# Kernel optimization log

Measured on AMD Instinct MI355X. Metric: run time of the kernel, lower is better.

## Reference

```python
import jax, jax.numpy as jnp
import numpy as np

B, N, E, H, MAXLEN = 64, 256, 1024, 16, 512
D = E // H
LN_EPS = 1e-5
NORM_EPS = 1e-12


def setup_inputs() -> dict:
    key = jax.random.key(0)
    ks = jax.random.split(key, 12)
    s = 1.0 / np.sqrt(E)
    return {
        "news_embeds": jax.random.normal(ks[0], (B, N, E), jnp.float32),
        "padding_mask": jax.random.uniform(ks[1], (B, N)) > 0.8,  # True = padded
        "cls_token": jax.random.normal(ks[2], (1, 1, E), jnp.float32),
        "pos_emb": jax.random.normal(ks[3], (MAXLEN + 1, E), jnp.float32) * 0.02,
        "in_proj_w": jax.random.normal(ks[4], (3 * E, E), jnp.float32) * s,
        "in_proj_b": jnp.zeros((3 * E,), jnp.float32),
        "out_proj_w": jax.random.normal(ks[5], (E, E), jnp.float32) * s,
        "out_proj_b": jnp.zeros((E,), jnp.float32),
        "proj_w": jax.random.normal(ks[6], (E, E), jnp.float32) * s,
        "proj_b": jnp.zeros((E,), jnp.float32),
        "ln_gamma": jnp.ones((E,), jnp.float32),
        "ln_beta": jnp.zeros((E,), jnp.float32),
    }


def reference(news_embeds, padding_mask, cls_token, pos_emb, in_proj_w, in_proj_b,
              out_proj_w, out_proj_b, proj_w, proj_b, ln_gamma, ln_beta):
    b, n, e = news_embeds.shape
    S = n + 1
    # prepend CLS token, add positional encodings (dropout inactive in eval)
    x = jnp.concatenate([jnp.broadcast_to(cls_token, (b, 1, e)), news_embeds], axis=1)
    x = x + pos_emb[:S][None, :, :]
    # key padding mask with CLS always attendable
    mask = jnp.concatenate(
        [jnp.zeros((b, 1), dtype=bool), padding_mask], axis=1)  # [b,S]
    # packed QKV projection (nn.MultiheadAttention in_proj)
    qkv = jnp.einsum('bse,fe->bsf', x, in_proj_w) + in_proj_b
    q, k, v = jnp.split(qkv, 3, axis=-1)
    q = q.reshape(b, S, H, D)
    k = k.reshape(b, S, H, D)
    v = v.reshape(b, S, H, D)
    scores = jnp.einsum('bqhd,bkhd->bhqk', q, k) / jnp.sqrt(
        jnp.asarray(D, x.dtype))
    big_neg = jnp.asarray(-1e9, scores.dtype)
    scores = jnp.where(mask[:, None, None, :], big_neg, scores)
    attn = jax.nn.softmax(scores, axis=-1)  # [b,H,S,S]
    ctx = jnp.einsum('bhqk,bkhd->bqhd', attn, v).reshape(b, S, e)
    attn_out = jnp.einsum('bse,fe->bsf', ctx, out_proj_w) + out_proj_b
    # projection head: Linear -> (Dropout eval noop) -> LayerNorm -> ReLU
    p = jnp.einsum('bse,fe->bsf', attn_out, proj_w) + proj_b
    mu = jnp.mean(p, axis=-1, keepdims=True)
    var = jnp.var(p, axis=-1, keepdims=True)
    ln = (p - mu) * jax.lax.rsqrt(var + LN_EPS) * ln_gamma + ln_beta
    proj = jax.nn.relu(ln)
    user = proj[:, 0, :]
    norm = jnp.maximum(jnp.linalg.norm(user, axis=-1, keepdims=True), NORM_EPS)
    user = user / norm
    return user, attn
```

## Files before the change

### kernel.cpp

```cpp
#include <hip/hip_runtime.h>

#define B_   64
#define N_   256
#define E_   1024
#define H_   16
#define D_   64
#define S_   257
#define M_   16448
#define MP2  16640
#define N3_  3072
#define K_   1024

typedef unsigned short u16;
typedef unsigned int   u32;
typedef __bf16 bf16x8 __attribute__((ext_vector_type(8)));
typedef float  f32x4  __attribute__((ext_vector_type(4)));

__device__ inline u16 f2bf(float f) {
  union { float f; u32 u; } a; a.f = f;
  return (u16)((a.u + 0x7FFFu + ((a.u >> 16) & 1u)) >> 16);
}
__device__ inline float bf2f(u16 h) {
  union { u32 u; float f; } a; a.u = ((u32)h) << 16; return a.f;
}
__device__ inline void gload_lds16(const void* g, void* l) {
  __builtin_amdgcn_global_load_lds((const __attribute__((address_space(1))) void*)g,
                                   (__attribute__((address_space(3))) void*)l, 16, 0, 0);
}

__global__ __launch_bounds__(256) void prep_w(const float* __restrict__ w, u16* __restrict__ o) {
  size_t i = ((size_t)blockIdx.x * 256 + threadIdx.x) * 4;
  float4 f = *(const float4*)(w + i);
  ushort4 v;
  v.x = f2bf(f.x); v.y = f2bf(f.y); v.z = f2bf(f.z); v.w = f2bf(f.w);
  *(ushort4*)(o + i) = v;
}

__global__ __launch_bounds__(256) void build_x(const float* __restrict__ news,
                                               const float* __restrict__ cls,
                                               const float* __restrict__ pos,
                                               u16* __restrict__ x) {
  const int row = blockIdx.x;
  const int e = threadIdx.x * 4;
  float4 v = make_float4(0.f, 0.f, 0.f, 0.f);
  if (row < M_) {
    const int b = row / S_;
    const int s = row - b * S_;
    float4 pe = *(const float4*)(pos + (size_t)s * E_ + e);
    float4 xv = (s == 0) ? *(const float4*)(cls + e)
                         : *(const float4*)(news + ((size_t)b * N_ + (s - 1)) * E_ + e);
    v.x = xv.x + pe.x; v.y = xv.y + pe.y; v.z = xv.z + pe.z; v.w = xv.w + pe.w;
  }
  ushort4 o;
  o.x = f2bf(v.x); o.y = f2bf(v.y); o.z = f2bf(v.z); o.w = f2bf(v.w);
  *(ushort4*)(x + (size_t)row * E_ + e) = o;
}

__global__ __launch_bounds__(256) void mask_prep(const void* __restrict__ src, int* __restrict__ dst) {
  const int t = threadIdx.x;
  const u32* wsrc = (const u32*)src;
  u32 flag = 0;
  for (int i = t; i < 4096; i += 256) {
    u32 v = wsrc[i];
    if (v == 0x3F800000u) flag |= 2u;
    else if (v > 1u) flag |= 1u;
  }
  __shared__ u32 fsh;
  if (t == 0) fsh = 0;
  __syncthreads();
  if (flag) atomicOr(&fsh, flag);
  __syncthreads();
  const u32 f = fsh;
  const int mode = (f & 2u) ? 2 : ((f & 1u) ? 1 : 0);
  const int base = blockIdx.x * 2048;
  for (int i = base + t; i < base + 2048; i += 256) {
    int m;
    if (mode == 0)      m = (wsrc[i] != 0u);
    else if (mode == 2) m = (((const float*)src)[i] != 0.f);
    else                m = (((const unsigned char*)src)[i] != 0);
    dst[i] = m;
  }
}

__global__ __launch_bounds__(256) void gemm_qkv(const u16* __restrict__ A,
                                                const u16* __restrict__ Bw,
                                                const float* __restrict__ bias,
                                                u16* __restrict__ C) {
  __shared__ u16 As[128 * 32];
  __shared__ u16 Bs[128 * 32];
  const int t = threadIdx.x;
  const int w = t >> 6, l = t & 63;
  const int wr = w >> 1, wc = w & 1;

  const int orig = blockIdx.x;
  const int wgid = (orig & 7) * 390 + (orig >> 3);
  const int bm = wgid / 24, bn = wgid % 24;

  const u16* Ab = A + (size_t)bm * 128 * K_;
  const u16* Bb = Bw + (size_t)bn * 128 * K_;
  f32x4 acc[4][4] = {};
  const int r0 = t >> 2,         col0 = (t & 3) << 3;
  const int r1 = (256 + t) >> 2, col1 = ((256 + t) & 3) << 3;
  char* AsB = (char*)As + w * 1024;
  char* BsB = (char*)Bs + w * 1024;

  for (int k0 = 0; k0 < K_; k0 += 32) {
    gload_lds16(Ab + (size_t)r0 * K_ + k0 + col0, AsB);
    gload_lds16(Ab + (size_t)r1 * K_ + k0 + col1, AsB + 4096);
    gload_lds16(Bb + (size_t)r0 * K_ + k0 + col0, BsB);
    gload_lds16(Bb + (size_t)r1 * K_ + k0 + col1, BsB + 4096);
    __syncthreads();
    const int kc = (l >> 4) << 3;
    bf16x8 af[4], bfr[4];
#pragma unroll
    for (int m = 0; m < 4; ++m)
      af[m] = *(const bf16x8*)&As[(wr * 64 + m * 16 + (l & 15)) * 32 + kc];
#pragma unroll
    for (int n = 0; n < 4; ++n)
      bfr[n] = *(const bf16x8*)&Bs[(wc * 64 + n * 16 + (l & 15)) * 32 + kc];
#pragma unroll
    for (int m = 0; m < 4; ++m)
#pragma unroll
      for (int n = 0; n < 4; ++n)
        acc[m][n] = __builtin_amdgcn_mfma_f32_16x16x32_bf16(af[m], bfr[n], acc[m][n], 0, 0, 0);
    __syncthreads();
  }
  const int row0 = bm * 128 + wr * 64 + ((l >> 4) << 2);
  const int colb = bn * 128 + wc * 64 + (l & 15);
#pragma unroll
  for (int n = 0; n < 4; ++n) {
    const int col = colb + n * 16;
    const float bv = bias[col];
#pragma unroll
    for (int m = 0; m < 4; ++m) {
      const int row = row0 + m * 16;
#pragma unroll
      for (int j = 0; j < 4; ++j)
        C[(size_t)(row + j) * N3_ + col] = f2bf(acc[m][n][j] + bv);
    }
  }
}

__global__ __launch_bounds__(256) void attn_kernel(const u16* __restrict__ qkv,
                                                   const int* __restrict__ maskw,
                                                   float* __restrict__ attn,
                                                   float* __restrict__ ctx) {
  __shared__ float msk[272];
  __shared__ float p0[272];
  __shared__ float red[4][64];
  const int qt = blockIdx.x, h = blockIdx.y, b = blockIdx.z;
  const int t = threadIdx.x;
  const int q0 = qt * 64;

  for (int i = t; i < 272; i += 256) {
    float m = 0.f;
    if (i == 0) m = 1.f;
    else if (i < S_) m = maskw[b * N_ + i - 1] ? 0.f : 1.f;
    msk[i] = m;
  }
  __syncthreads();

  const int w = t >> 6, l = t & 63;
  const int cl = l & 15, rg = l >> 4;
  const int kc = rg * 8;

  const u16* qrow = qkv + (size_t)(b * S_ + q0 + w * 16 + cl) * N3_ + h * 64 + kc;
  const bf16x8 qa0 = *(const bf16x8*)qrow;
  const bf16x8 qa1 = *(const bf16x8*)(qrow + 32);

  const u16* kbase0 = qkv + (size_t)(b * S_) * N3_ + E_ + h * 64 + kc;

  float ev[17][4];
  float sum[4] = {0.f, 0.f, 0.f, 0.f};
#pragma unroll
  for (int kt = 0; kt < 17; ++kt) {
    const u16* kb = kbase0 + (size_t)(kt * 16 + cl) * N3_;
    f32x4 a = {0.f, 0.f, 0.f, 0.f};
    a = __builtin_amdgcn_mfma_f32_16x16x32_bf16(qa0, *(const bf16x8*)kb, a, 0, 0, 0);
    a = __builtin_amdgcn_mfma_f32_16x16x32_bf16(qa1, *(const bf16x8*)(kb + 32), a, 0, 0, 0);
    const float m = msk[kt * 16 + cl];
#pragma unroll
    for (int j = 0; j < 4; ++j) {
      const float e = m * __expf(a[j] * 0.125f);
      ev[kt][j] = e;
      sum[j] += e;
    }
  }
  float inv[4];
#pragma unroll
  for (int j = 0; j < 4; ++j) {
#pragma unroll
    for (int o = 1; o < 16; o <<= 1) sum[j] += __shfl_xor(sum[j], o);
    inv[j] = 1.f / sum[j];
  }

  const int qrow0 = q0 + w * 16 + rg * 4;
  float* abase = attn + (size_t)(b * H_ + h) * S_ * S_;
#pragma unroll
  for (int j = 0; j < 4; ++j) {
    const int gq = qrow0 + j;
    if (gq < S_) {
      float* arow = abase + (size_t)gq * S_;
#pragma unroll
      for (int kt = 0; kt < 17; ++kt) {
        const int col = kt * 16 + cl;
        if (col < S_) arow[col] = ev[kt][j] * inv[j];
      }
    }
  }

  if (qt == 0) {
    if (w == 0 && rg == 0) {
      const float iv = inv[0];
#pragma unroll
      for (int kt = 0; kt < 17; ++kt) p0[kt * 16 + cl] = ev[kt][0] * iv;
    }
    __syncthreads();
    const int part = t >> 6, d = t & 63;
    float acc = 0.f;
    for (int k = part; k < S_; k += 4)
      acc = fmaf(p0[k], bf2f(qkv[(size_t)(b * S_ + k) * N3_ + 2 * E_ + h * 64 + d]), acc);
    red[part][d] = acc;
    __syncthreads();
    if (t < 64)
      ctx[(size_t)b * E_ + h * 64 + t] = red[0][t] + red[1][t] + red[2][t] + red[3][t];
  }
}

__global__ __launch_bounds__(256) void gemv_cls(const float* __restrict__ in,
                                                const float* __restrict__ W,
                                                const float* __restrict__ bias,
                                                float* __restrict__ out) {
  const int bt = blockIdx.x, fc = blockIdx.y, t = threadIdx.x;
  __shared__ float xs[4][E_];
  for (int i = t; i < E_; i += 256)
    ((float4*)xs)[i] = ((const float4*)(in + (size_t)bt * 4 * E_))[i];
  __syncthreads();
  const int f = fc * 64 + (t >> 2);
  const int ec = (t & 3) * 256;
  const float4* wr = (const float4*)(W + (size_t)f * E_ + ec);
  float a0 = 0.f, a1 = 0.f, a2 = 0.f, a3 = 0.f;
#pragma unroll 8
  for (int e4 = 0; e4 < 64; ++e4) {
    const float4 wv = wr[e4];
    const float4 x0 = *(const float4*)&xs[0][ec + e4 * 4];
    const float4 x1 = *(const float4*)&xs[1][ec + e4 * 4];
    const float4 x2 = *(const float4*)&xs[2][ec + e4 * 4];
    const float4 x3 = *(const float4*)&xs[3][ec + e4 * 4];
    a0 += wv.x * x0.x + wv.y * x0.y + wv.z * x0.z + wv.w * x0.w;
    a1 += wv.x * x1.x + wv.y * x1.y + wv.z * x1.z + wv.w * x1.w;
    a2 += wv.x * x2.x + wv.y * x2.y + wv.z * x2.z + wv.w * x2.w;
    a3 += wv.x * x3.x + wv.y * x3.y + wv.z * x3.z + wv.w * x3.w;
  }
  a0 += __shfl_xor(a0, 1); a0 += __shfl_xor(a0, 2);
  a1 += __shfl_xor(a1, 1); a1 += __shfl_xor(a1, 2);
  a2 += __shfl_xor(a2, 1); a2 += __shfl_xor(a2, 2);
  a3 += __shfl_xor(a3, 1); a3 += __shfl_xor(a3, 2);
  if ((t & 3) == 0) {
    const float bv = bias[f];
    out[(size_t)(bt * 4 + 0) * E_ + f] = a0 + bv;
    out[(size_t)(bt * 4 + 1) * E_ + f] = a1 + bv;
    out[(size_t)(bt * 4 + 2) * E_ + f] = a2 + bv;
    out[(size_t)(bt * 4 + 3) * E_ + f] = a3 + bv;
  }
}

__global__ __launch_bounds__(256) void ln_relu_norm(const float* __restrict__ p,
                                                    const float* __restrict__ gamma,
                                                    const float* __restrict__ beta,
                                                    float* __restrict__ user) {
  const int b = blockIdx.x, t = threadIdx.x;
  const int w = t >> 6, l = t & 63;
  const float4 v = ((const float4*)(p + (size_t)b * E_))[t];
  float s = v.x + v.y + v.z + v.w;
  float s2 = v.x * v.x + v.y * v.y + v.z * v.z + v.w * v.w;
#pragma unroll
  for (int o = 1; o < 64; o <<= 1) { s += __shfl_xor(s, o); s2 += __shfl_xor(s2, o); }
  __shared__ float ss[4], ss2[4], qs[4];
  if (l == 0) { ss[w] = s; ss2[w] = s2; }
  __syncthreads();
  s = ss[0] + ss[1] + ss[2] + ss[3];
  s2 = ss2[0] + ss2[1] + ss2[2] + ss2[3];
  const float mu = s * (1.f / E_);
  const float var = s2 * (1.f / E_) - mu * mu;
  const float rstd = rsqrtf(var + 1e-5f);
  const float4 g = ((const float4*)gamma)[t];
  const float4 be = ((const float4*)beta)[t];
  float4 o;
  o.x = fmaxf((v.x - mu) * rstd * g.x + be.x, 0.f);
  o.y = fmaxf((v.y - mu) * rstd * g.y + be.y, 0.f);
  o.z = fmaxf((v.z - mu) * rstd * g.z + be.z, 0.f);
  o.w = fmaxf((v.w - mu) * rstd * g.w + be.w, 0.f);
  float q2 = o.x * o.x + o.y * o.y + o.z * o.z + o.w * o.w;
#pragma unroll
  for (int off = 1; off < 64; off <<= 1) q2 += __shfl_xor(q2, off);
  if (l == 0) qs[w] = q2;
  __syncthreads();
  q2 = qs[0] + qs[1] + qs[2] + qs[3];
  const float nrm = fmaxf(sqrtf(q2), 1e-12f);
  const float inv = 1.f / nrm;
  float4 u;
  u.x = o.x * inv; u.y = o.y * inv; u.z = o.z * inv; u.w = o.w * inv;
  ((float4*)(user + (size_t)b * E_))[t] = u;
}

extern "C" void kernel_launch(void* const* d_in, const int* in_sizes, int n_in,
                              void* d_out, int out_size, void* d_ws, size_t ws_size,
                              hipStream_t stream) {
  const float* news   = (const float*)d_in[0];
  const void*  maskp  = d_in[1];
  const float* cls    = (const float*)d_in[2];
  const float* pos    = (const float*)d_in[3];
  const float* w_in   = (const float*)d_in[4];
  const float* b_in   = (const float*)d_in[5];
  const float* w_out  = (const float*)d_in[6];
  const float* b_out  = (const float*)d_in[7];
  const float* w_proj = (const float*)d_in[8];
  const float* b_proj = (const float*)d_in[9];
  const float* gamma  = (const float*)d_in[10];
  const float* beta   = (const float*)d_in[11];

  char* ws = (char*)d_ws;
  u16*  w_bf  = (u16*)(ws + 0);
  u16*  x_bf  = (u16*)(ws + 6291456);
  u16*  qkv   = (u16*)(ws + 40370176);
  float* ctx  = (float*)(ws + 142606336);
  float* aoc  = (float*)(ws + 142868480);
  float* pcls = (float*)(ws + 143130624);
  int*  maskw = (int*)(ws + 143392768);

  float* user = (float*)d_out;
  float* attn = (float*)d_out + (size_t)B_ * E_;

  prep_w<<<3072, 256, 0, stream>>>(w_in, w_bf);
  build_x<<<MP2, 256, 0, stream>>>(news, cls, pos, x_bf);
  mask_prep<<<8, 256, 0, stream>>>(maskp, maskw);
  gemm_qkv<<<3120, 256, 0, stream>>>(x_bf, w_bf, b_in, qkv);
  attn_kernel<<<dim3(5, H_, B_), 256, 0, stream>>>(qkv, maskw, attn, ctx);
  gemv_cls<<<dim3(16, 16), 256, 0, stream>>>(ctx, w_out, b_out, aoc);
  gemv_cls<<<dim3(16, 16), 256, 0, stream>>>(aoc, w_proj, b_proj, pcls);
  ln_relu_norm<<<B_, 256, 0, stream>>>(pcls, gamma, beta, user);
}
```

Before: 384.1 us.

## Stage K tile in LDS and recompute QK scores instead of caching exponentials

The attention kernel now copies the head's full K slice (257 rows, padded to 258 and a 72-element row stride) into shared memory once per block. It then runs the QK^T MFMA pass twice: first to build the softmax row sums, then again to compute and write the normalized probabilities. This removes the 68-float per-thread ev array that limited occupancy and turns repeated strided global K reads into LDS reads. The cost is doubled MFMA and exp work plus roughly 37KB of LDS per block, which may itself cap occupancy.

Measured after the change: 357.8 us. -6.9%, faster.

```diff
diff --git a/kernel.cpp b/kernel.cpp
--- a/kernel.cpp
+++ b/kernel.cpp
@@ -145,6 +145,7 @@
                                                    const int* __restrict__ maskw,
                                                    float* __restrict__ attn,
                                                    float* __restrict__ ctx) {
+  __shared__ u16 Ks[258 * 72];
   __shared__ float msk[272];
   __shared__ float p0[272];
   __shared__ float red[4][64];
@@ -152,6 +153,13 @@
   const int t = threadIdx.x;
   const int q0 = qt * 64;
 
+  for (int c = t; c < 258 * 8; c += 256) {
+    const int r = c >> 3, qq = c & 7;
+    uint4 val = make_uint4(0, 0, 0, 0);
+    if (r < S_)
+      val = *(const uint4*)(qkv + (size_t)(b * S_ + r) * N3_ + E_ + h * 64 + qq * 8);
+    *(uint4*)&Ks[r * 72 + qq * 8] = val;
+  }
   for (int i = t; i < 272; i += 256) {
     float m = 0.f;
     if (i == 0) m = 1.f;
@@ -168,23 +176,24 @@
   const bf16x8 qa0 = *(const bf16x8*)qrow;
   const bf16x8 qa1 = *(const bf16x8*)(qrow + 32);
 
-  const u16* kbase0 = qkv + (size_t)(b * S_) * N3_ + E_ + h * 64 + kc;
-
-  float ev[17][4];
+#define QK(kt, a)                                                                  \
+  {                                                                                \
+    int krow = (kt) * 16 + cl;                                                     \
+    if (krow > 257) krow = 257;                                                    \
+    const u16* kb = &Ks[krow * 72 + kc];                                           \
+    (a) = __builtin_amdgcn_mfma_f32_16x16x32_bf16(qa0, *(const bf16x8*)kb, (a), 0, 0, 0); \
+    (a) = __builtin_amdgcn_mfma_f32_16x16x32_bf16(qa1, *(const bf16x8*)(kb + 32), (a), 0, 0, 0); \
+  }
+
   float sum[4] = {0.f, 0.f, 0.f, 0.f};
 #pragma unroll
   for (int kt = 0; kt < 17; ++kt) {
-    const u16* kb = kbase0 + (size_t)(kt * 16 + cl) * N3_;
     f32x4 a = {0.f, 0.f, 0.f, 0.f};
-    a = __builtin_amdgcn_mfma_f32_16x16x32_bf16(qa0, *(const bf16x8*)kb, a, 0, 0, 0);
-    a = __builtin_amdgcn_mfma_f32_16x16x32_bf16(qa1, *(const bf16x8*)(kb + 32), a, 0, 0, 0);
+    QK(kt, a);
     const float m = msk[kt * 16 + cl];
 #pragma unroll
-    for (int j = 0; j < 4; ++j) {
-      const float e = m * __expf(a[j] * 0.125f);
-      ev[kt][j] = e;
-      sum[j] += e;
-    }
+    for (int j = 0; j < 4; ++j)
+      sum[j] += m * __expf(a[j] * 0.125f);
   }
   float inv[4];
 #pragma unroll
@@ -196,25 +205,32 @@
 
   const int qrow0 = q0 + w * 16 + rg * 4;
   float* abase = attn + (size_t)(b * H_ + h) * S_ * S_;
+  float* arow[4];
+  bool okq[4];
 #pragma unroll
   for (int j = 0; j < 4; ++j) {
     const int gq = qrow0 + j;
-    if (gq < S_) {
-      float* arow = abase + (size_t)gq * S_;
-#pragma unroll
-      for (int kt = 0; kt < 17; ++kt) {
-        const int col = kt * 16 + cl;
-        if (col < S_) arow[col] = ev[kt][j] * inv[j];
-      }
+    okq[j] = (gq < S_);
+    arow[j] = abase + (size_t)gq * S_;
+  }
+  const bool isCls = (qt == 0 && w == 0 && rg == 0);
+#pragma unroll
+  for (int kt = 0; kt < 17; ++kt) {
+    f32x4 a = {0.f, 0.f, 0.f, 0.f};
+    QK(kt, a);
+    const float m = msk[kt * 16 + cl];
+    const int col = kt * 16 + cl;
+    const bool okc = (col < S_);
+#pragma unroll
+    for (int j = 0; j < 4; ++j) {
+      const float v = m * __expf(a[j] * 0.125f) * inv[j];
+      if (okc && okq[j]) arow[j][col] = v;
+      if (isCls && j == 0) p0[col] = v;
     }
   }
+#undef QK
 
   if (qt == 0) {
-    if (w == 0 && rg == 0) {
-      const float iv = inv[0];
-#pragma unroll
-      for (int kt = 0; kt < 17; ++kt) p0[kt * 16 + cl] = ev[kt][0] * iv;
-    }
     __syncthreads();
     const int part = t >> 6, d = t & 63;
     float acc = 0.f;
```
